# Kernel tuning notes

Measured on AMD Instinct MI355X. Metric: run time of the kernel, lower is better.

Reference implementation:

```python
import jax, jax.numpy as jnp
import numpy as np

N_NODES = 50000
SEQ = 12
CH = 128
BS = 4

def setup_inputs() -> dict:
    key = jax.random.key(0)
    k1, k2, k3, k4, k5 = jax.random.split(key, 5)
    x = jax.random.normal(k1, (BS, N_NODES, CH), dtype=jnp.float32)
    indices = jax.random.randint(k2, (N_NODES, SEQ), 0, N_NODES)
    # xavier-uniform-like init for per-node spiral weights [n_nodes, seq]
    bound = float(np.sqrt(6.0 / (N_NODES + SEQ)))
    weight = jax.random.uniform(k3, (N_NODES, SEQ), minval=-bound, maxval=bound, dtype=jnp.float32)
    gate_w = jax.random.normal(k4, (CH, CH), dtype=jnp.float32) * (1.0 / np.sqrt(CH))
    gate_b = jax.random.normal(k5, (CH,), dtype=jnp.float32) * 0.01
    return {"x": x, "indices": indices, "weight": weight, "gate_w": gate_w, "gate_b": gate_b}

def reference(x, indices, weight, gate_w, gate_b):
    # gate projection: [bs, n, ch]
    gate = jnp.einsum('bnc,dc->bnd', x, gate_w) + gate_b
    # gather spiral neighbors along node axis: [bs, n*s, ch] -> [bs, n, s, ch]
    gathered = jnp.take(x, indices.reshape(-1), axis=1)
    gathered = gathered.reshape(x.shape[0], indices.shape[0], indices.shape[1], x.shape[2])
    # per-node weighted reduction over spiral positions
    out = jnp.einsum('bvsf,vs->bvf', gathered, weight)
    return out * gate
```

## Files before the change

### kernel.cpp

```cpp
#include <hip/hip_runtime.h>
#include <hip/hip_bf16.h>

#define N_NODES 50000
#define SEQ 12
#define CH 128
#define BS 4
#define TILE 64
#define PAD_ROW 132
#define NTILES ((N_NODES + TILE - 1) / TILE)

#define NODES_PER_WAVE 16
#define CHUNK_NODES 2
#define CHUNK_FLOATS (CHUNK_NODES * SEQ * CH)
#define NCHUNK (NODES_PER_WAVE / CHUNK_NODES)

typedef short bf16x8 __attribute__((ext_vector_type(8)));
typedef float f32x4 __attribute__((ext_vector_type(4)));

__device__ __forceinline__ void gload_lds16(const float* g, float* l) {
    __builtin_amdgcn_global_load_lds(
        (const __attribute__((address_space(1))) void*)g,
        (__attribute__((address_space(3))) void*)l,
        16, 0, 0);
}

__global__ __launch_bounds__(256, 1) void gated_spiral_async(
    const float* __restrict__ x,
    const int* __restrict__ indices,
    const float* __restrict__ weight,
    const float* __restrict__ gate_w,
    const float* __restrict__ gate_b,
    float* __restrict__ out)
{
    __shared__ float spiral[TILE * PAD_ROW];
    __shared__ float gbuf[4][2][CHUNK_FLOATS];
    __shared__ int   idx_s[TILE * SEQ];
    __shared__ float w_s[TILE * SEQ];

    const int tid  = threadIdx.x;
    const int wave = tid >> 6;
    const int lane = tid & 63;
    const int b    = blockIdx.y;
    const int node0 = blockIdx.x * TILE;
    const float* xb = x + (size_t)b * N_NODES * CH;

    const int sbase = wave * NODES_PER_WAVE * SEQ;
    #pragma unroll
    for (int k3 = 0; k3 < 3; ++k3) {
        const int k = k3 * 64 + lane;
        int node = node0 + wave * NODES_PER_WAVE + k / SEQ;
        if (node >= N_NODES) node = N_NODES - 1;
        int t = indices[(size_t)node * SEQ + (k % SEQ)];
        t = t < 0 ? 0 : (t >= N_NODES ? N_NODES - 1 : t);
        idx_s[sbase + k] = t;
        w_s[sbase + k]   = weight[(size_t)node * SEQ + (k % SEQ)];
    }

    {
        const int n  = lane >> 5;
        const int co = (lane & 31) * 4;
        const int* idxw = idx_s + sbase;
        const float* ww = w_s + sbase;
        float* gb0 = &gbuf[wave][0][0];

        #pragma unroll
        for (int c0 = 0; c0 < 2; ++c0) {
            const int* ix = idxw + c0 * CHUNK_NODES * SEQ;
            float* dst = gb0 + c0 * CHUNK_FLOATS;
            #pragma unroll
            for (int s = 0; s < SEQ; ++s) {
                const int row = ix[n * SEQ + s];
                gload_lds16(xb + (size_t)row * CH + co, dst + s * (CHUNK_NODES * CH));
            }
        }

        #pragma unroll
        for (int c = 0; c < NCHUNK; ++c) {
            if (c < NCHUNK - 1) asm volatile("s_waitcnt vmcnt(12)" ::: "memory");
            else                asm volatile("s_waitcnt vmcnt(0)"  ::: "memory");
            __builtin_amdgcn_sched_barrier(0);

            float* cur = gb0 + (c & 1) * CHUNK_FLOATS;
            const float* wp = ww + c * CHUNK_NODES * SEQ + n * SEQ;
            float a0 = 0.f, a1 = 0.f, a2 = 0.f, a3 = 0.f;
            #pragma unroll
            for (int s = 0; s < SEQ; ++s) {
                const float4 d = *(const float4*)(cur + (s * CHUNK_NODES + n) * CH + co);
                const float ws = wp[s];
                a0 += ws * d.x; a1 += ws * d.y; a2 += ws * d.z; a3 += ws * d.w;
            }
            const int r = wave * NODES_PER_WAVE + c * CHUNK_NODES + n;
            *(float4*)(spiral + r * PAD_ROW + co) = make_float4(a0, a1, a2, a3);

            if (c + 2 < NCHUNK) {
                asm volatile("s_waitcnt lgkmcnt(0)" ::: "memory");
                __builtin_amdgcn_sched_barrier(0);
                const int* ix = idxw + (c + 2) * CHUNK_NODES * SEQ;
                #pragma unroll
                for (int s = 0; s < SEQ; ++s) {
                    const int row = ix[n * SEQ + s];
                    gload_lds16(xb + (size_t)row * CH + co, cur + s * (CHUNK_NODES * CH));
                }
            }
        }
    }

    {
        const int m = lane & 15;
        const int quad = lane >> 4;

        int arow_node = node0 + wave * 16 + m;
        if (arow_node >= N_NODES) arow_node = N_NODES - 1;
        const float* ap = xb + (size_t)arow_node * CH + quad * 8;

        bf16x8 afrag[4];
        #pragma unroll
        for (int kk = 0; kk < 4; ++kk) {
            float4 lo = *(const float4*)(ap + kk * 32);
            float4 hi = *(const float4*)(ap + kk * 32 + 4);
            union { bf16x8 v; __hip_bfloat16 h[8]; } af;
            af.h[0] = __float2bfloat16(lo.x); af.h[1] = __float2bfloat16(lo.y);
            af.h[2] = __float2bfloat16(lo.z); af.h[3] = __float2bfloat16(lo.w);
            af.h[4] = __float2bfloat16(hi.x); af.h[5] = __float2bfloat16(hi.y);
            af.h[6] = __float2bfloat16(hi.z); af.h[7] = __float2bfloat16(hi.w);
            afrag[kk] = af.v;
        }

        float gbv[8];
        #pragma unroll
        for (int t = 0; t < 8; ++t)
            gbv[t] = gate_b[t * 16 + m];

        #pragma unroll
        for (int t = 0; t < 8; ++t) {
            f32x4 c = {0.f, 0.f, 0.f, 0.f};
            const float* bp = gate_w + (size_t)(t * 16 + m) * CH + quad * 8;
            #pragma unroll
            for (int kk = 0; kk < 4; ++kk) {
                float4 lo = *(const float4*)(bp + kk * 32);
                float4 hi = *(const float4*)(bp + kk * 32 + 4);
                union { bf16x8 v; __hip_bfloat16 h[8]; } bf;
                bf.h[0] = __float2bfloat16(lo.x); bf.h[1] = __float2bfloat16(lo.y);
                bf.h[2] = __float2bfloat16(lo.z); bf.h[3] = __float2bfloat16(lo.w);
                bf.h[4] = __float2bfloat16(hi.x); bf.h[5] = __float2bfloat16(hi.y);
                bf.h[6] = __float2bfloat16(hi.z); bf.h[7] = __float2bfloat16(hi.w);
                c = __builtin_amdgcn_mfma_f32_16x16x32_bf16(afrag[kk], bf.v, c, 0, 0, 0);
            }
            #pragma unroll
            for (int reg = 0; reg < 4; ++reg) {
                const int r = wave * 16 + quad * 4 + reg;
                const int col = t * 16 + m;
                const float sp = spiral[r * PAD_ROW + col];
                spiral[r * PAD_ROW + col] = sp * (c[reg] + gbv[t]);
            }
        }
    }

    {
        #pragma unroll
        for (int p = 0; p < 8; ++p) {
            const int seg = p * 64 + lane;
            const int r = seg >> 5;
            const int c4 = (seg & 31) * 4;
            const int node = node0 + wave * 16 + r;
            if (node < N_NODES) {
                const float* sp = spiral + (wave * 16 + r) * PAD_ROW + c4;
                f32x4 v = { sp[0], sp[1], sp[2], sp[3] };
                __builtin_nontemporal_store(v, (f32x4*)(out + ((size_t)b * N_NODES + node) * CH + c4));
            }
        }
    }
}

extern "C" void kernel_launch(void* const* d_in, const int* in_sizes, int n_in,
                              void* d_out, int out_size, void* d_ws, size_t ws_size,
                              hipStream_t stream) {
    const float* x       = (const float*)d_in[0];
    const int*   indices = (const int*)d_in[1];
    const float* weight  = (const float*)d_in[2];
    const float* gate_w  = (const float*)d_in[3];
    const float* gate_b  = (const float*)d_in[4];
    float*       out     = (float*)d_out;

    dim3 grid(NTILES, BS);
    gated_spiral_async<<<grid, dim3(256), 0, stream>>>(
        x, indices, weight, gate_w, gate_b, out);
}
```

Before: 400.4 us.

## Pre-convert x to bf16 and split channels into halves for spiral gather

Adds a conversion kernel that writes x as bf16 into the workspace, then runs a new spiral kernel that gathers bf16 rows. Each block handles one 64-channel half for a batch/tile group, with the batch and half folded into blockIdx.x. Halving the gathered bytes and the per-block LDS footprint is meant to cut the random-gather memory traffic and allow two blocks per CU. The cost is an extra full pass over x (read fp32, write bf16) and reduced precision in the spiral sum. The old fp32 kernel is kept as a fallback when the workspace is too small.

```diff
diff --git a/kernel.cpp b/kernel.cpp
--- a/kernel.cpp
+++ b/kernel.cpp
@@ -6,23 +6,207 @@
 #define CH 128
 #define BS 4
 #define TILE 64
+#define NTILES ((N_NODES + TILE - 1) / TILE)
+#define HALF 64
+#define PAD_S 68
 #define PAD_ROW 132
-#define NTILES ((N_NODES + TILE - 1) / TILE)
-
-#define NODES_PER_WAVE 16
-#define CHUNK_NODES 2
-#define CHUNK_FLOATS (CHUNK_NODES * SEQ * CH)
-#define NCHUNK (NODES_PER_WAVE / CHUNK_NODES)
+
+#define CNODES 4
+#define NCHUNK 4
+#define CHUNK_SHORTS (CNODES * SEQ * HALF)
+#define CHUNK_INSTR (CHUNK_SHORTS / 512)
 
 typedef short bf16x8 __attribute__((ext_vector_type(8)));
 typedef float f32x4 __attribute__((ext_vector_type(4)));
 
-__device__ __forceinline__ void gload_lds16(const float* g, float* l) {
+__device__ __forceinline__ float bflo(unsigned int u) { return __uint_as_float(u << 16); }
+__device__ __forceinline__ float bfhi(unsigned int u) { return __uint_as_float(u & 0xFFFF0000u); }
+
+__device__ __forceinline__ void gload_lds16b(const unsigned short* g, unsigned short* l) {
     __builtin_amdgcn_global_load_lds(
         (const __attribute__((address_space(1))) void*)g,
         (__attribute__((address_space(3))) void*)l,
         16, 0, 0);
 }
+__device__ __forceinline__ void gload_lds16f(const float* g, float* l) {
+    __builtin_amdgcn_global_load_lds(
+        (const __attribute__((address_space(1))) void*)g,
+        (__attribute__((address_space(3))) void*)l,
+        16, 0, 0);
+}
+
+__global__ __launch_bounds__(256) void convert_kernel(
+    const float* __restrict__ x,
+    unsigned short* __restrict__ xb)
+{
+    const size_t i = (size_t)blockIdx.x * 256 + threadIdx.x;
+    const size_t n8 = (size_t)BS * N_NODES * CH / 8;
+    if (i < n8) {
+        float4 lo = *(const float4*)(x + i * 8);
+        float4 hi = *(const float4*)(x + i * 8 + 4);
+        union { bf16x8 v; __hip_bfloat16 h[8]; } o;
+        o.h[0] = __float2bfloat16(lo.x); o.h[1] = __float2bfloat16(lo.y);
+        o.h[2] = __float2bfloat16(lo.z); o.h[3] = __float2bfloat16(lo.w);
+        o.h[4] = __float2bfloat16(hi.x); o.h[5] = __float2bfloat16(hi.y);
+        o.h[6] = __float2bfloat16(hi.z); o.h[7] = __float2bfloat16(hi.w);
+        *(bf16x8*)(xb + i * 8) = o.v;
+    }
+}
+
+__global__ __launch_bounds__(256, 2) void gated_spiral_slice(
+    const unsigned short* __restrict__ xb,
+    const int* __restrict__ indices,
+    const float* __restrict__ weight,
+    const float* __restrict__ gate_w,
+    const float* __restrict__ gate_b,
+    float* __restrict__ out)
+{
+    __shared__ float spiral[TILE * PAD_S];
+    __shared__ unsigned short gbuf[4][2][CHUNK_SHORTS];
+    __shared__ int   idx_s[TILE * SEQ];
+    __shared__ float w_s[TILE * SEQ];
+
+    const int tid  = threadIdx.x;
+    const int wave = tid >> 6;
+    const int lane = tid & 63;
+
+    const int grp  = blockIdx.x & 7;
+    const int b    = grp >> 1;
+    const int half = grp & 1;
+    const int tile = blockIdx.x >> 3;
+    const int node0 = tile * TILE;
+    const unsigned short* xbb = xb + (size_t)b * N_NODES * CH;
+
+    const int sbase = wave * 16 * SEQ;
+    #pragma unroll
+    for (int k3 = 0; k3 < 3; ++k3) {
+        const int k = k3 * 64 + lane;
+        int node = node0 + wave * 16 + k / SEQ;
+        if (node >= N_NODES) node = N_NODES - 1;
+        int t = indices[(size_t)node * SEQ + (k % SEQ)];
+        t = t < 0 ? 0 : (t >= N_NODES ? N_NODES - 1 : t);
+        idx_s[sbase + k] = t;
+        w_s[sbase + k]   = weight[(size_t)node * SEQ + (k % SEQ)];
+    }
+
+    {
+        const int* idxw = idx_s + sbase;
+        const float* ww = w_s + sbase;
+        unsigned short* gw0 = &gbuf[wave][0][0];
+        const int lrs = lane >> 3;
+        const int lco = (lane & 7) * 8;
+
+        #pragma unroll
+        for (int c0 = 0; c0 < 2; ++c0) {
+            unsigned short* dst = gw0 + c0 * CHUNK_SHORTS;
+            #pragma unroll
+            for (int i = 0; i < CHUNK_INSTR; ++i) {
+                const int rs = i * 8 + lrs;
+                const int s = rs >> 2, n = rs & 3;
+                const int row = idxw[(c0 * CNODES + n) * SEQ + s];
+                gload_lds16b(xbb + (size_t)row * CH + half * HALF + lco, dst + i * 512);
+            }
+        }
+
+        #pragma unroll
+        for (int c = 0; c < NCHUNK; ++c) {
+            if (c < NCHUNK - 1) asm volatile("s_waitcnt vmcnt(6)" ::: "memory");
+            else                asm volatile("s_waitcnt vmcnt(0)" ::: "memory");
+            __builtin_amdgcn_sched_barrier(0);
+
+            unsigned short* bufp = gw0 + (c & 1) * CHUNK_SHORTS;
+            const int nr = lane >> 4;
+            const int cc = (lane & 15) * 4;
+            const float* wp = ww + (c * CNODES + nr) * SEQ;
+            float a0 = 0.f, a1 = 0.f, a2 = 0.f, a3 = 0.f;
+            #pragma unroll
+            for (int s = 0; s < SEQ; ++s) {
+                const uint2 d = *(const uint2*)(bufp + (s * 4 + nr) * HALF + cc);
+                const float ws = wp[s];
+                a0 += ws * bflo(d.x); a1 += ws * bfhi(d.x);
+                a2 += ws * bflo(d.y); a3 += ws * bfhi(d.y);
+            }
+            const int r = wave * 16 + c * CNODES + nr;
+            *(float4*)(spiral + r * PAD_S + cc) = make_float4(a0, a1, a2, a3);
+
+            if (c + 2 < NCHUNK) {
+                asm volatile("s_waitcnt lgkmcnt(0)" ::: "memory");
+                __builtin_amdgcn_sched_barrier(0);
+                #pragma unroll
+                for (int i = 0; i < CHUNK_INSTR; ++i) {
+                    const int rs = i * 8 + lrs;
+                    const int s = rs >> 2, n = rs & 3;
+                    const int row = idxw[((c + 2) * CNODES + n) * SEQ + s];
+                    gload_lds16b(xbb + (size_t)row * CH + half * HALF + lco, bufp + i * 512);
+                }
+            }
+        }
+    }
+
+    {
+        const int m = lane & 15;
+        const int quad = lane >> 4;
+
+        int arow_node = node0 + wave * 16 + m;
+        if (arow_node >= N_NODES) arow_node = N_NODES - 1;
+        const unsigned short* ap = xbb + (size_t)arow_node * CH + quad * 8;
+
+        bf16x8 afrag[4];
+        #pragma unroll
+        for (int kk = 0; kk < 4; ++kk)
+            afrag[kk] = *(const bf16x8*)(ap + kk * 32);
+
+        float gbv[4];
+        #pragma unroll
+        for (int t = 0; t < 4; ++t)
+            gbv[t] = gate_b[half * HALF + t * 16 + m];
+
+        #pragma unroll
+        for (int t = 0; t < 4; ++t) {
+            f32x4 c = {0.f, 0.f, 0.f, 0.f};
+            const float* bp = gate_w + (size_t)(half * HALF + t * 16 + m) * CH + quad * 8;
+            #pragma unroll
+            for (int kk = 0; kk < 4; ++kk) {
+                float4 lo = *(const float4*)(bp + kk * 32);
+                float4 hi = *(const float4*)(bp + kk * 32 + 4);
+                union { bf16x8 v; __hip_bfloat16 h[8]; } bf;
+                bf.h[0] = __float2bfloat16(lo.x); bf.h[1] = __float2bfloat16(lo.y);
+                bf.h[2] = __float2bfloat16(lo.z); bf.h[3] = __float2bfloat16(lo.w);
+                bf.h[4] = __float2bfloat16(hi.x); bf.h[5] = __float2bfloat16(hi.y);
+                bf.h[6] = __float2bfloat16(hi.z); bf.h[7] = __float2bfloat16(hi.w);
+                c = __builtin_amdgcn_mfma_f32_16x16x32_bf16(afrag[kk], bf.v, c, 0, 0, 0);
+            }
+            #pragma unroll
+            for (int reg = 0; reg < 4; ++reg) {
+                const int r = wave * 16 + quad * 4 + reg;
+                const int col = t * 16 + m;
+                const float sp = spiral[r * PAD_S + col];
+                spiral[r * PAD_S + col] = sp * (c[reg] + gbv[t]);
+            }
+        }
+    }
+
+    {
+        #pragma unroll
+        for (int p = 0; p < 4; ++p) {
+            const int seg = p * 64 + lane;
+            const int r = seg >> 4;
+            const int cc = (seg & 15) * 4;
+            const int node = node0 + wave * 16 + r;
+            if (node < N_NODES) {
+                const float* sp = spiral + (wave * 16 + r) * PAD_S + cc;
+                f32x4 v = { sp[0], sp[1], sp[2], sp[3] };
+                __builtin_nontemporal_store(v,
+                    (f32x4*)(out + ((size_t)b * N_NODES + node) * CH + half * HALF + cc));
+            }
+        }
+    }
+}
+
+#define NODES_PER_WAVE 16
+#define FCHUNK_NODES 2
+#define FCHUNK_FLOATS (FCHUNK_NODES * SEQ * CH)
+#define FNCHUNK (NODES_PER_WAVE / FCHUNK_NODES)
 
 __global__ __launch_bounds__(256, 1) void gated_spiral_async(
     const float* __restrict__ x,
@@ -33,7 +217,7 @@
     float* __restrict__ out)
 {
     __shared__ float spiral[TILE * PAD_ROW];
-    __shared__ float gbuf[4][2][CHUNK_FLOATS];
+    __shared__ float gbuf[4][2][FCHUNK_FLOATS];
     __shared__ int   idx_s[TILE * SEQ];
     __shared__ float w_s[TILE * SEQ];
 
@@ -65,41 +249,41 @@
 
         #pragma unroll
         for (int c0 = 0; c0 < 2; ++c0) {
-            const int* ix = idxw + c0 * CHUNK_NODES * SEQ;
-            float* dst = gb0 + c0 * CHUNK_FLOATS;
+            const int* ix = idxw + c0 * FCHUNK_NODES * SEQ;
+            float* dst = gb0 + c0 * FCHUNK_FLOATS;
             #pragma unroll
             for (int s = 0; s < SEQ; ++s) {
                 const int row = ix[n * SEQ + s];
-                gload_lds16(xb + (size_t)row * CH + co, dst + s * (CHUNK_NODES * CH));
-            }
-        }
-
-        #pragma unroll
-        for (int c = 0; c < NCHUNK; ++c) {
-            if (c < NCHUNK - 1) asm volatile("s_waitcnt vmcnt(12)" ::: "memory");
-            else                asm volatile("s_waitcnt vmcnt(0)"  ::: "memory");
+                gload_lds16f(xb + (size_t)row * CH + co, dst + s * (FCHUNK_NODES * CH));
+            }
+        }
+
+        #pragma unroll
+        for (int c = 0; c < FNCHUNK; ++c) {
+            if (c < FNCHUNK - 1) asm volatile("s_waitcnt vmcnt(12)" ::: "memory");
+            else                 asm volatile("s_waitcnt vmcnt(0)"  ::: "memory");
             __builtin_amdgcn_sched_barrier(0);
 
-            float* cur = gb0 + (c & 1) * CHUNK_FLOATS;
-            const float* wp = ww + c * CHUNK_NODES * SEQ + n * SEQ;
+            float* cur = gb0 + (c & 1) * FCHUNK_FLOATS;
+            const float* wp = ww + c * FCHUNK_NODES * SEQ + n * SEQ;
             float a0 = 0.f, a1 = 0.f, a2 = 0.f, a3 = 0.f;
             #pragma unroll
             for (int s = 0; s < SEQ; ++s) {
-                const float4 d = *(const float4*)(cur + (s * CHUNK_NODES + n) * CH + co);
+                const float4 d = *(const float4*)(cur + (s * FCHUNK_NODES + n) * CH + co);
                 const float ws = wp[s];
                 a0 += ws * d.x; a1 += ws * d.y; a2 += ws * d.z; a3 += ws * d.w;
             }
-            const int r = wave * NODES_PER_WAVE + c * CHUNK_NODES + n;
+            const int r = wave * NODES_PER_WAVE + c * FCHUNK_NODES + n;
             *(float4*)(spiral + r * PAD_ROW + co) = make_float4(a0, a1, a2, a3);
 
-            if (c + 2 < NCHUNK) {
+            if (c + 2 < FNCHUNK) {
                 asm volatile("s_waitcnt lgkmcnt(0)" ::: "memory");
                 __builtin_amdgcn_sched_barrier(0);
-                const int* ix = idxw + (c + 2) * CHUNK_NODES * SEQ;
+                const int* ix = idxw + (c + 2) * FCHUNK_NODES * SEQ;
                 #pragma unroll
                 for (int s = 0; s < SEQ; ++s) {
                     const int row = ix[n * SEQ + s];
-                    gload_lds16(xb + (size_t)row * CH + co, cur + s * (CHUNK_NODES * CH));
+                    gload_lds16f(xb + (size_t)row * CH + co, cur + s * (FCHUNK_NODES * CH));
                 }
             }
         }
@@ -182,7 +366,17 @@
     const float* gate_b  = (const float*)d_in[4];
     float*       out     = (float*)d_out;
 
-    dim3 grid(NTILES, BS);
-    gated_spiral_async<<<grid, dim3(256), 0, stream>>>(
-        x, indices, weight, gate_w, gate_b, out);
-}
+    const size_t x_bf_bytes = (size_t)BS * N_NODES * CH * 2;
+
+    if (ws_size >= x_bf_bytes) {
+        unsigned short* xbuf = (unsigned short*)d_ws;
+        const size_t n8 = (size_t)BS * N_NODES * CH / 8;
+        convert_kernel<<<dim3((unsigned)((n8 + 255) / 256)), dim3(256), 0, stream>>>(x, xbuf);
+        gated_spiral_slice<<<dim3(NTILES * 8), dim3(256), 0, stream>>>(
+            xbuf, indices, weight, gate_w, gate_b, out);
+    } else {
+        dim3 grid(NTILES, BS);
+        gated_spiral_async<<<grid, dim3(256), 0, stream>>>(
+            x, indices, weight, gate_w, gate_b, out);
+    }
+}
```

After: 324.2 us. -19.0%, faster.
